# Optimization experiments

Measured on AMD Instinct MI355X. Metric: run time of the kernel, lower is better.

The kernel has to match this reference:

```python
import jax, jax.numpy as jnp
import numpy as np

B, S, D_IN = 2, 2048, 1024
H = 16
HD = 64  # head_dim = d_out // head_cnt


def setup_inputs() -> dict:
    key = jax.random.key(0)
    kx, kq, kk, kv = jax.random.split(key, 4)
    x = jax.random.normal(kx, (B, S, D_IN), dtype=jnp.float32)
    # Per-head Q/K/V projection weights, stacked: [H, d_in, head_dim].
    # Matches nn.Linear(d_in, head_out) per head (qkv_bias=False), scaled like
    # a typical init.
    sc = 1.0 / np.sqrt(D_IN)
    Wq = jax.random.normal(kq, (H, D_IN, HD), dtype=jnp.float32) * sc
    Wk = jax.random.normal(kk, (H, D_IN, HD), dtype=jnp.float32) * sc
    Wv = jax.random.normal(kv, (H, D_IN, HD), dtype=jnp.float32) * sc
    return {"x": x, "Wq": Wq, "Wk": Wk, "Wv": Wv}


def reference(x, Wq, Wk, Wv):
    # Batched multi-head causal attention equivalent to the per-head loop +
    # torch.cat(dim=-1): head h's output occupies slice [h*HD:(h+1)*HD].
    q = jnp.einsum("bsd,hde->bhse", x, Wq)  # [B,H,S,HD]
    k = jnp.einsum("bsd,hde->bhse", x, Wk)
    v = jnp.einsum("bsd,hde->bhse", x, Wv)
    scale = 1.0 / jnp.sqrt(jnp.asarray(HD, dtype=x.dtype))
    scores = jnp.einsum("bhse,bhte->bhst", q, k) * scale  # [B,H,S,S]
    seq = x.shape[1]
    causal = jnp.tril(jnp.ones((seq, seq), dtype=bool))
    scores = jnp.where(causal, scores, jnp.asarray(-jnp.inf, dtype=scores.dtype))
    attn = jax.nn.softmax(scores, axis=-1)  # dropout = 0.0 -> identity
    ctx = jnp.einsum("bhst,bhte->bhse", attn, v)  # [B,H,S,HD]
    # concat heads on last dim
    b, h, s, e = ctx.shape
    return ctx.transpose(0, 2, 1, 3).reshape(b, s, h * e)
```

## Files before the change

### kernel.cpp

```cpp
#include <hip/hip_runtime.h>


#define DI   1024
#define HD   64
#define NH   16
#define SEQ  2048
#define NB   2

typedef unsigned short u16;
typedef unsigned short us8 __attribute__((ext_vector_type(8)));
typedef unsigned short us4 __attribute__((ext_vector_type(4)));
typedef unsigned int   u32x2 __attribute__((ext_vector_type(2)));
typedef short bf8 __attribute__((ext_vector_type(8)));
typedef float f4 __attribute__((ext_vector_type(4)));

#define MFMA16(a, b, c) __builtin_amdgcn_mfma_f32_16x16x32_bf16((a), (b), (c), 0, 0, 0)

#if __has_builtin(__builtin_amdgcn_exp2f)
#define EXP2(x) __builtin_amdgcn_exp2f(x)
#else
#define EXP2(x) exp2f(x)
#endif

#if __has_builtin(__builtin_amdgcn_perm)
#define PKHI(a, b) __builtin_amdgcn_perm((a), (b), 0x07060302u)
#else
__device__ __forceinline__ unsigned PKHI(unsigned a, unsigned b) {
  return (b >> 16) | (a & 0xffff0000u);
}
#endif

__device__ __forceinline__ u16 f2bf(float f) {
  unsigned u = __float_as_uint(f);
  u += 0x7fffu + ((u >> 16) & 1u);
  return (u16)(u >> 16);
}

__device__ __forceinline__ void async16(const u16* g, u16* l) {
  __builtin_amdgcn_global_load_lds((const __attribute__((address_space(1))) void*)g,
                                   (__attribute__((address_space(3))) void*)l,
                                   16, 0, 0);
}

__global__ __launch_bounds__(256) void prep_k(const float* __restrict__ x,
                                              const float* __restrict__ Wq,
                                              const float* __restrict__ Wk,
                                              const float* __restrict__ Wv,
                                              u16* __restrict__ xb,
                                              u16* __restrict__ Wt) {
  __shared__ __align__(16) u16 tile[64][72];
  const int bid = blockIdx.x;
  if (bid < 2048) {
    const int i = (bid * 256 + threadIdx.x) * 8;
    float4 v0 = *(const float4*)(x + i);
    float4 v1 = *(const float4*)(x + i + 4);
    us8 o;
    o[0] = f2bf(v0.x); o[1] = f2bf(v0.y); o[2] = f2bf(v0.z); o[3] = f2bf(v0.w);
    o[4] = f2bf(v1.x); o[5] = f2bf(v1.y); o[6] = f2bf(v1.z); o[7] = f2bf(v1.w);
    *(us8*)(xb + i) = o;
    return;
  }
  const int idx = bid - 2048;
  const int mh = idx >> 4;
  const int d0 = (idx & 15) * 64;
  const int mat = mh >> 4, h = mh & 15;
  const float* W = (mat == 0 ? Wq : (mat == 1 ? Wk : Wv)) + (size_t)h * DI * HD;
  const int t = threadIdx.x;
  {
    const int r = t >> 2, c = (t & 3) * 16;
    const float* src = W + (size_t)(d0 + r) * HD + c;
    #pragma unroll
    for (int j = 0; j < 4; j++) {
      float4 v = *(const float4*)(src + j * 4);
      tile[r][c + j * 4 + 0] = f2bf(v.x);
      tile[r][c + j * 4 + 1] = f2bf(v.y);
      tile[r][c + j * 4 + 2] = f2bf(v.z);
      tile[r][c + j * 4 + 3] = f2bf(v.w);
    }
  }
  __syncthreads();
  {
    const int e = t >> 2, c = (t & 3) * 16;
    __align__(16) u16 tmp[16];
    #pragma unroll
    for (int i = 0; i < 16; i++) tmp[i] = tile[c + i][e];
    u16* dst = Wt + ((size_t)mh * HD + e) * DI + d0 + c;
    *(us8*)dst       = *(us8*)&tmp[0];
    *(us8*)(dst + 8) = *(us8*)&tmp[8];
  }
}

__global__ __launch_bounds__(256) void proj_k(const u16* __restrict__ x,
                                              const u16* __restrict__ Wt,
                                              u16* __restrict__ Qo,
                                              u16* __restrict__ Ko,
                                              u16* __restrict__ Vo) {
  __shared__ __align__(16) u16 xs[128 * 64];
  __shared__ __align__(16) u16 ws[128 * 64];
  const int m0 = blockIdx.x * 128, n0 = blockIdx.y * 128;
  const int tid = threadIdx.x, w = tid >> 6, lane = tid & 63;
  const int l15 = lane & 15, quad = lane >> 4;
  const int lrow = lane >> 3, lch = lane & 7;
  const int l7 = l15 & 7;

  f4 acc[4][4];
  #pragma unroll
  for (int i = 0; i < 4; i++)
    #pragma unroll
    for (int j = 0; j < 4; j++) {
      f4 z = {0.f, 0.f, 0.f, 0.f};
      acc[i][j] = z;
    }

  const u16* xg = x  + (size_t)(m0 + lrow) * DI + ((lch ^ lrow) * 8);
  const u16* wg = Wt + (size_t)(n0 + lrow) * DI + ((lch ^ lrow) * 8);

  for (int k0 = 0; k0 < DI; k0 += 64) {
    #pragma unroll
    for (int i = 0; i < 4; i++) {
      const int r0 = i * 32 + w * 8;
      async16(xg + (size_t)r0 * DI + k0, &xs[r0 * 64]);
      async16(wg + (size_t)r0 * DI + k0, &ws[r0 * 64]);
    }
    __syncthreads();
    #pragma unroll
    for (int ks = 0; ks < 64; ks += 32) {
      const int c0 = (ks >> 3) + quad;
      bf8 af[4], bfr[4];
      #pragma unroll
      for (int i = 0; i < 4; i++)
        af[i] = *(const bf8*)&xs[((w >> 1) * 64 + i * 16 + l15) * 64 + ((c0 ^ l7) * 8)];
      #pragma unroll
      for (int i = 0; i < 4; i++)
        bfr[i] = *(const bf8*)&ws[((w & 1) * 64 + i * 16 + l15) * 64 + ((c0 ^ l7) * 8)];
      #pragma unroll
      for (int mi = 0; mi < 4; mi++)
        #pragma unroll
        for (int ni = 0; ni < 4; ni++)
          acc[mi][ni] = MFMA16(af[mi], bfr[ni], acc[mi][ni]);
    }
    __syncthreads();
  }

  const int mat = n0 >> 10;
  const int nf0 = n0 + (w & 1) * 64;
  const float qscale = 0.125f * 1.44269504088896340736f;
  #pragma unroll
  for (int mi = 0; mi < 4; mi++) {
    const int mrow = m0 + (w >> 1) * 64 + mi * 16 + quad * 4;
    const int b = mrow >> 11, sb = mrow & (SEQ - 1);
    #pragma unroll
    for (int ni = 0; ni < 4; ni++) {
      const int nf = nf0 + ni * 16;
      const int h = (nf >> 6) & 15;
      const int e = (nf & 63) + l15;
      if (mat == 2) {
        __align__(8) u16 pk[4];
        #pragma unroll
        for (int r = 0; r < 4; r++) pk[r] = f2bf(acc[mi][ni][r]);
        *(us4*)(Vo + (((size_t)b * NH + h) * HD + e) * SEQ + sb) = *(us4*)pk;
      } else {
        u16* O = mat ? Ko : Qo;
        const float sc = mat ? 1.0f : qscale;
        #pragma unroll
        for (int r = 0; r < 4; r++)
          O[(((size_t)b * NH + h) * SEQ + sb + r) * HD + e] = f2bf(acc[mi][ni][r] * sc);
      }
    }
  }
}

__global__ __launch_bounds__(256, 2) void attn_k(const u16* __restrict__ Qo,
                                                 const u16* __restrict__ Ko,
                                                 const u16* __restrict__ Vo,
                                                 float* __restrict__ out) {
  __shared__ __align__(16) u16 Ks[128 * 64];
  __shared__ __align__(16) u16 Vs[64 * 128];
  __shared__ __align__(16) u16 PsA[4][16][136];
  __shared__ __align__(16) u16 PsB[4][16][136];
  const int ia = blockIdx.x;
  const int ib = 31 - ia;
  const int bh = blockIdx.y;
  const int b = bh >> 4, h = bh & 15;
  const int tid = threadIdx.x, w = tid >> 6, lane = tid & 63;
  const int l15 = lane & 15, quad = lane >> 4;

  const u16* Qb = Qo + (size_t)bh * SEQ * HD;
  const u16* Kb = Ko + (size_t)bh * SEQ * HD;
  const u16* Vb = Vo + (size_t)bh * HD * SEQ;

  const int qrowA = ia * 64 + w * 16 + l15;
  const int qrowB = ib * 64 + w * 16 + l15;
  bf8 bqA0 = *(const bf8*)(Qb + (size_t)qrowA * HD + quad * 8);
  bf8 bqA1 = *(const bf8*)(Qb + (size_t)qrowA * HD + 32 + quad * 8);
  bf8 bqB0 = *(const bf8*)(Qb + (size_t)qrowB * HD + quad * 8);
  bf8 bqB1 = *(const bf8*)(Qb + (size_t)qrowB * HD + 32 + quad * 8);

  f4 oA[4], oB[4], lA, lB;
  #pragma unroll
  for (int i = 0; i < 4; i++) {
    f4 z = {0.f, 0.f, 0.f, 0.f};
    oA[i] = z; oB[i] = z;
  }
  {
    f4 z = {0.f, 0.f, 0.f, 0.f};
    lA = z; lB = z;
  }
  const bf8 ones = {0x3F80, 0x3F80, 0x3F80, 0x3F80, 0x3F80, 0x3F80, 0x3F80, 0x3F80};

  const int nA = ia / 2 + 1, nB = ib / 2 + 1;

  const u16* ksp0 = &Ks[l15 * 64 + ((quad ^ (l15 & 7)) * 8)];
  const u16* ksp1 = &Ks[l15 * 64 + (((quad + 4) ^ (l15 & 7)) * 8)];
  const u16* vsp[4];
  #pragma unroll
  for (int tc = 0; tc < 4; tc++)
    vsp[tc] = &Vs[l15 * 128 + (((tc * 4 + quad) ^ l15) * 8)];
  u16* pwA = &PsA[w][l15][quad * 4];
  u16* pwB = &PsB[w][l15][quad * 4];
  const u16* prA = &PsA[w][l15][quad * 8];
  const u16* prB = &PsB[w][l15][quad * 8];

  const int kl = lane >> 3, kc = lane & 7;
  const int vl = lane >> 4, vc = lane & 15;
  const u16* kg = Kb + (size_t)(w * 32 + kl) * HD + ((kc ^ kl) * 8);
  const u16* vg[4];
  u16* ldsK[4];
  u16* ldsV[4];
  #pragma unroll
  for (int i = 0; i < 4; i++) {
    const int vr = w * 16 + i * 4;
    const int f = (i * 4 + vl) & 15;
    vg[i] = Vb + (size_t)(vr + vl) * SEQ + ((vc ^ f) * 8);
    ldsK[i] = &Ks[(w * 32 + i * 8) * 64];
    ldsV[i] = &Vs[vr * 128];
  }

  const int mqA = qrowA - (nA - 1) * 128 - quad * 4;
  const int mqB = qrowB - (nB - 1) * 128 - quad * 4;

  auto pphase = [&](f4* s, u16* pw, bool domask, int mq) {
    #pragma unroll
    for (int mf = 0; mf < 8; mf++) {
      f4 sv = s[mf];
      if (domask) {
        #pragma unroll
        for (int r = 0; r < 4; r++)
          sv[r] = (mf * 16 + r <= mq) ? sv[r] : -1e30f;
      }
      const unsigned p0 = __float_as_uint(EXP2(sv[0]));
      const unsigned p1 = __float_as_uint(EXP2(sv[1]));
      const unsigned p2 = __float_as_uint(EXP2(sv[2]));
      const unsigned p3 = __float_as_uint(EXP2(sv[3]));
      u32x2 pk = {PKHI(p1, p0), PKHI(p3, p2)};
      *(u32x2*)(pw + mf * 16) = pk;
    }
  };

  for (int it = 0; it < nB; it++) {
    #pragma unroll
    for (int i = 0; i < 4; i++) {
      async16(kg + i * 512, ldsK[i]);
      async16(vg[i], ldsV[i]);
    }
    __syncthreads();
    const bool doA = (it < nA);

    f4 sA[8], sB[8];
    #pragma unroll
    for (int mf = 0; mf < 8; mf++) {
      bf8 ak0 = *(const bf8*)(ksp0 + mf * 1024);
      bf8 ak1 = *(const bf8*)(ksp1 + mf * 1024);
      f4 z = {0.f, 0.f, 0.f, 0.f};
      f4 tb = MFMA16(ak0, bqB0, z);
      sB[mf] = MFMA16(ak1, bqB1, tb);
      if (doA) {
        f4 ta = MFMA16(ak0, bqA0, z);
        sA[mf] = MFMA16(ak1, bqA1, ta);
      }
    }

    pphase(sB, pwB, it == nB - 1, mqB);
    if (doA) pphase(sA, pwA, it == nA - 1, mqA);

    #pragma unroll
    for (int tc = 0; tc < 4; tc++) {
      bf8 pfB = *(const bf8*)(prB + tc * 32);
      lB = MFMA16(ones, pfB, lB);
      bf8 pfA;
      if (doA) {
        pfA = *(const bf8*)(prA + tc * 32);
        lA = MFMA16(ones, pfA, lA);
      }
      #pragma unroll
      for (int ef = 0; ef < 4; ef++) {
        bf8 vf = *(const bf8*)(vsp[tc] + ef * 2048);
        oB[ef] = MFMA16(vf, pfB, oB[ef]);
        if (doA) oA[ef] = MFMA16(vf, pfA, oA[ef]);
      }
    }
    __syncthreads();
    kg += 128 * HD;
    #pragma unroll
    for (int i = 0; i < 4; i++) vg[i] += 128;
  }

  const float invA = 1.0f / lA[0];
  const float invB = 1.0f / lB[0];
  float* opA = out + ((size_t)b * SEQ + qrowA) * (NH * HD) + h * HD + quad * 4;
  float* opB = out + ((size_t)b * SEQ + qrowB) * (NH * HD) + h * HD + quad * 4;
  #pragma unroll
  for (int ef = 0; ef < 4; ef++) {
    f4 va = oA[ef] * invA;
    f4 vb = oB[ef] * invB;
    *(float4*)(opA + ef * 16) = *(float4*)&va;
    *(float4*)(opB + ef * 16) = *(float4*)&vb;
  }
}

extern "C" void kernel_launch(void* const* d_in, const int* in_sizes, int n_in,
                              void* d_out, int out_size, void* d_ws, size_t ws_size,
                              hipStream_t stream) {
  const float* x  = (const float*)d_in[0];
  const float* Wq = (const float*)d_in[1];
  const float* Wk = (const float*)d_in[2];
  const float* Wv = (const float*)d_in[3];
  float* out = (float*)d_out;

  u16* xb = (u16*)d_ws;
  u16* Wt = xb + (size_t)NB * SEQ * DI;
  u16* Qo = Wt + (size_t)3 * NH * HD * DI;
  u16* Ko = Qo + (size_t)NB * NH * SEQ * HD;
  u16* Vo = Ko + (size_t)NB * NH * SEQ * HD;

  prep_k<<<dim3(2048 + 768), 256, 0, stream>>>(x, Wq, Wk, Wv, xb, Wt);
  proj_k<<<dim3(32, 24), 256, 0, stream>>>(xb, Wt, Qo, Ko, Vo);
  attn_k<<<dim3(16, 32), 256, 0, stream>>>(Qo, Ko, Vo, out);
}
```

Baseline: 161.6 us.

## Double-buffer K/V tiles in LDS and share a swizzled P buffer between query tiles

The K and V LDS tiles become double-buffered. The next tile's async loads are issued right after the barrier, so global-to-LDS transfer overlaps compute, and one of the two barriers per iteration is removed. The two per-query-tile P buffers become a single XOR-swizzled P buffer that the B and A tiles use in turn. This doubles K/V shared memory but drops the padded P arrays, and it serializes the A and B PV phases, which may reduce interleaving of MFMAs. Reusing Ps for A right after B relies on intra-wave ordering with no barrier.

Result: faster. 158.4 us (-2.0%).

```diff
diff --git a/kernel.cpp b/kernel.cpp
--- a/kernel.cpp
+++ b/kernel.cpp
@@ -174,16 +174,16 @@
                                                  const u16* __restrict__ Ko,
                                                  const u16* __restrict__ Vo,
                                                  float* __restrict__ out) {
-  __shared__ __align__(16) u16 Ks[128 * 64];
-  __shared__ __align__(16) u16 Vs[64 * 128];
-  __shared__ __align__(16) u16 PsA[4][16][136];
-  __shared__ __align__(16) u16 PsB[4][16][136];
+  __shared__ __align__(16) u16 Ks[2 * 128 * 64];
+  __shared__ __align__(16) u16 Vs[2 * 64 * 128];
+  __shared__ __align__(16) u16 Ps[4 * 16 * 128];
   const int ia = blockIdx.x;
   const int ib = 31 - ia;
   const int bh = blockIdx.y;
   const int b = bh >> 4, h = bh & 15;
   const int tid = threadIdx.x, w = tid >> 6, lane = tid & 63;
   const int l15 = lane & 15, quad = lane >> 4;
+  const int qh = quad >> 1, ql = quad & 1;
 
   const u16* Qb = Qo + (size_t)bh * SEQ * HD;
   const u16* Kb = Ko + (size_t)bh * SEQ * HD;
@@ -216,10 +216,11 @@
   #pragma unroll
   for (int tc = 0; tc < 4; tc++)
     vsp[tc] = &Vs[l15 * 128 + (((tc * 4 + quad) ^ l15) * 8)];
-  u16* pwA = &PsA[w][l15][quad * 4];
-  u16* pwB = &PsB[w][l15][quad * 4];
-  const u16* prA = &PsA[w][l15][quad * 8];
-  const u16* prB = &PsB[w][l15][quad * 8];
+  u16* const psw = &Ps[w * 2048 + l15 * 128 + ql * 4];
+  const u16* prp[4];
+  #pragma unroll
+  for (int tc = 0; tc < 4; tc++)
+    prp[tc] = &Ps[w * 2048 + l15 * 128 + (((tc * 4 + quad) ^ l15) * 8)];
 
   const int kl = lane >> 3, kc = lane & 7;
   const int vl = lane >> 4, vc = lane & 15;
@@ -239,7 +240,7 @@
   const int mqA = qrowA - (nA - 1) * 128 - quad * 4;
   const int mqB = qrowB - (nB - 1) * 128 - quad * 4;
 
-  auto pphase = [&](f4* s, u16* pw, bool domask, int mq) {
+  auto pphase = [&](f4* s, bool domask, int mq) {
     #pragma unroll
     for (int mf = 0; mf < 8; mf++) {
       f4 sv = s[mf];
@@ -253,24 +254,40 @@
       const unsigned p2 = __float_as_uint(EXP2(sv[2]));
       const unsigned p3 = __float_as_uint(EXP2(sv[3]));
       u32x2 pk = {PKHI(p1, p0), PKHI(p3, p2)};
-      *(u32x2*)(pw + mf * 16) = pk;
+      *(u32x2*)(psw + ((((mf << 1) | qh) ^ l15) * 8)) = pk;
     }
   };
 
+  #pragma unroll
+  for (int i = 0; i < 4; i++) {
+    async16(kg + i * 512, ldsK[i]);
+    async16(vg[i], ldsV[i]);
+  }
+  kg += 128 * HD;
+  #pragma unroll
+  for (int i = 0; i < 4; i++) vg[i] += 128;
+
   for (int it = 0; it < nB; it++) {
-    #pragma unroll
-    for (int i = 0; i < 4; i++) {
-      async16(kg + i * 512, ldsK[i]);
-      async16(vg[i], ldsV[i]);
-    }
+    const int cb = (it & 1) * 8192;
     __syncthreads();
+    if (it + 1 < nB) {
+      const int nb = 8192 - cb;
+      #pragma unroll
+      for (int i = 0; i < 4; i++) {
+        async16(kg + i * 512, ldsK[i] + nb);
+        async16(vg[i], ldsV[i] + nb);
+      }
+      kg += 128 * HD;
+      #pragma unroll
+      for (int i = 0; i < 4; i++) vg[i] += 128;
+    }
     const bool doA = (it < nA);
 
     f4 sA[8], sB[8];
     #pragma unroll
     for (int mf = 0; mf < 8; mf++) {
-      bf8 ak0 = *(const bf8*)(ksp0 + mf * 1024);
-      bf8 ak1 = *(const bf8*)(ksp1 + mf * 1024);
+      bf8 ak0 = *(const bf8*)(ksp0 + cb + mf * 1024);
+      bf8 ak1 = *(const bf8*)(ksp1 + cb + mf * 1024);
       f4 z = {0.f, 0.f, 0.f, 0.f};
       f4 tb = MFMA16(ak0, bqB0, z);
       sB[mf] = MFMA16(ak1, bqB1, tb);
@@ -280,29 +297,30 @@
       }
     }
 
-    pphase(sB, pwB, it == nB - 1, mqB);
-    if (doA) pphase(sA, pwA, it == nA - 1, mqA);
-
+    pphase(sB, it == nB - 1, mqB);
     #pragma unroll
     for (int tc = 0; tc < 4; tc++) {
-      bf8 pfB = *(const bf8*)(prB + tc * 32);
-      lB = MFMA16(ones, pfB, lB);
-      bf8 pfA;
-      if (doA) {
-        pfA = *(const bf8*)(prA + tc * 32);
-        lA = MFMA16(ones, pfA, lA);
-      }
+      bf8 pf = *(const bf8*)(prp[tc]);
+      lB = MFMA16(ones, pf, lB);
       #pragma unroll
       for (int ef = 0; ef < 4; ef++) {
-        bf8 vf = *(const bf8*)(vsp[tc] + ef * 2048);
-        oB[ef] = MFMA16(vf, pfB, oB[ef]);
-        if (doA) oA[ef] = MFMA16(vf, pfA, oA[ef]);
-      }
-    }
-    __syncthreads();
-    kg += 128 * HD;
-    #pragma unroll
-    for (int i = 0; i < 4; i++) vg[i] += 128;
+        bf8 vf = *(const bf8*)(vsp[tc] + cb + ef * 2048);
+        oB[ef] = MFMA16(vf, pf, oB[ef]);
+      }
+    }
+    if (doA) {
+      pphase(sA, it == nA - 1, mqA);
+      #pragma unroll
+      for (int tc = 0; tc < 4; tc++) {
+        bf8 pf = *(const bf8*)(prp[tc]);
+        lA = MFMA16(ones, pf, lA);
+        #pragma unroll
+        for (int ef = 0; ef < 4; ef++) {
+          bf8 vf = *(const bf8*)(vsp[tc] + cb + ef * 2048);
+          oA[ef] = MFMA16(vf, pf, oA[ef]);
+        }
+      }
+    }
   }
 
   const float invA = 1.0f / lA[0];
```
